# Performance work log

Measured on AMD Instinct MI355X. Metric: run time of the kernel, lower is better.

The kernel has to match this reference:

```python
import jax, jax.numpy as jnp
import numpy as np

N_HEAD = 16
DIM_K = 64
DIM_MODEL = N_HEAD * DIM_K  # 1024; seq_len is forced to equal dim_model by the reshape
SCALE = float(DIM_K ** 0.5)


def setup_inputs() -> dict:
    key = jax.random.key(0)
    ks = jax.random.split(key, 4)
    B, S, D = 32, DIM_MODEL, 1024
    x = jax.random.normal(ks[0], (B, S, D), dtype=jnp.float32)
    glorot = float(1.0 / np.sqrt(D))
    Wq = jax.random.normal(ks[1], (D, DIM_MODEL), dtype=jnp.float32) * glorot
    Wk = jax.random.normal(ks[2], (D, DIM_MODEL), dtype=jnp.float32) * glorot
    Wv = jax.random.normal(ks[3], (D, DIM_MODEL), dtype=jnp.float32) * glorot
    bq = jnp.zeros((DIM_MODEL,), jnp.float32)
    bk = jnp.zeros((DIM_MODEL,), jnp.float32)
    bv = jnp.zeros((DIM_MODEL,), jnp.float32)
    return {"x": x, "Wq": Wq, "bq": bq, "Wk": Wk, "bk": bk, "Wv": Wv, "bv": bv}


def reference(x, Wq, bq, Wk, bk, Wv, bv):
    # x: [B, S, D] with S == DIM_MODEL (required by the original reshape)
    B = x.shape[0]
    q = x @ Wq + bq  # [B, S, dm]
    k = x @ Wk + bk
    v = x @ Wv + bv
    # TF1 K.batch_dot(q, k, axes=[-1,-1]) -> tf.matmul(q, k, adjoint_a=True):
    # contracts over the SEQUENCE axis -> [B, dm, dm]
    y = jnp.einsum('bsd,bse->bde', q, k) / SCALE
    # softmax over dim_k-sized chunks of the last axis
    y = y.reshape(B, DIM_MODEL, N_HEAD, DIM_K)
    y = jax.nn.softmax(y, axis=-1)
    y = y.reshape(B, DIM_MODEL, DIM_MODEL)
    # TF1 K.batch_dot(v, y, axes=[2,3]) -> tf.matmul(v, y) (no adjoints)
    out = jnp.einsum('bsd,bde->bse', v, y)  # [B, S, dm]
    return out
```

## Files before the change

kernel.cpp:

```cpp
#include <hip/hip_runtime.h>
#include <hip/hip_bf16.h>

#define DM 1024
#define NB 32

typedef __bf16 bf16_t;
typedef __attribute__((ext_vector_type(8))) __bf16 bf16x8;
typedef __attribute__((ext_vector_type(4))) float  f32x4;

typedef __attribute__((address_space(1))) void gas_void;
typedef __attribute__((address_space(3))) void las_void;

__device__ __forceinline__ void async_lds16(const bf16_t* g, bf16_t* l) {
    __builtin_amdgcn_global_load_lds((gas_void*)g, (las_void*)l, 16, 0, 0);
}

__device__ inline float bf2f(bf16_t v) {
    union { unsigned short s; __bf16 b; } u; u.b = v;
    union { unsigned int i; float f; } w; w.i = ((unsigned int)u.s) << 16;
    return w.f;
}
__device__ inline bf16_t f2bf(float f) {
    union { unsigned int i; float f; } w; w.f = f;
    unsigned int r = (w.i + 0x7FFFu + ((w.i >> 16) & 1u)) >> 16;
    union { unsigned short s; __bf16 b; } u; u.s = (unsigned short)r;
    return u.b;
}

enum EpiMode { EPI_NONE = 0, EPI_BIAS_ROW = 1, EPI_BIAS_COL = 2, EPI_SCALE = 3 };

__global__ void detect_mode(const unsigned short* __restrict__ x, int* __restrict__ mode)
{
    if (threadIdx.x == 0 && blockIdx.x == 0) {
        int hits = 0;
        for (int i = 0; i < 2048; ++i) {
            unsigned e = (x[i] >> 7) & 0xFFu;
            hits += (e >= 0x8Du) ? 1 : 0;
        }
        *mode = (hits >= 16) ? 1 : 0;
    }
}

__global__ void convert_x(const void* __restrict__ xin, bf16_t* __restrict__ xb,
                          const int* __restrict__ modep, long long off, long long n8)
{
    const long long i = (long long)blockIdx.x * blockDim.x + threadIdx.x;
    if (i >= n8) return;
    bf16x8 o;
    if (*modep) {
        const float* s = (const float*)xin + off + i * 8;
#pragma unroll
        for (int j = 0; j < 8; ++j) o[j] = f2bf(s[j]);
    } else {
        o = *(const bf16x8*)((const bf16_t*)xin + off + i * 8);
    }
    *(bf16x8*)(xb + i * 8) = o;
}

__global__ void transpose3(const void* __restrict__ Wq, const void* __restrict__ Wk,
                           const void* __restrict__ Wv, bf16_t* __restrict__ Wt,
                           const int* __restrict__ modep)
{
    const int md = *modep;
    const void* src = (blockIdx.z == 0) ? Wq : (blockIdx.z == 1) ? Wk : Wv;
    bf16_t* dst = Wt + (size_t)blockIdx.z * DM * DM;
    __shared__ bf16_t T[64][72];
    const int tid = threadIdx.x;
    const int r  = tid >> 2;
    const int cp = tid & 3;
    const int r0 = blockIdx.y * 64;
    const int c0 = blockIdx.x * 64;
    const size_t base = (size_t)(r0 + r) * DM + c0 + cp * 16;
    bf16_t tmp[16];
    if (md) {
        const float* s = (const float*)src + base;
#pragma unroll
        for (int j = 0; j < 16; ++j) tmp[j] = f2bf(s[j]);
    } else {
        const bf16_t* s = (const bf16_t*)src + base;
        bf16x8 a = *(const bf16x8*)s;
        bf16x8 b = *(const bf16x8*)(s + 8);
#pragma unroll
        for (int j = 0; j < 8; ++j) { tmp[j] = a[j]; tmp[8 + j] = b[j]; }
    }
#pragma unroll
    for (int j = 0; j < 16; ++j) T[cp * 16 + j][r] = tmp[j];
    __syncthreads();
    bf16_t* d = dst + (size_t)(c0 + r) * DM + r0 + cp * 16;
    bf16x8 w0, w1;
#pragma unroll
    for (int j = 0; j < 8; ++j) w0[j] = T[r][cp * 16 + j];
#pragma unroll
    for (int j = 0; j < 8; ++j) w1[j] = T[r][cp * 16 + 8 + j];
    *(bf16x8*)d = w0;
    *(bf16x8*)(d + 8) = w1;
}

template <int MODE, bool DUALOUT>
__global__ __launch_bounds__(256, 2)
void gemm_nt(const bf16_t* __restrict__ A, long long sA,
             const bf16_t* __restrict__ B, long long sB,
             void* __restrict__ C, long long sC, long long cOff,
             const void* __restrict__ bias, const int* __restrict__ modep,
             int M, int N, int K, float scale)
{
    constexpr int BM = 128, BN = 128, BK = 64;
    __shared__ __align__(16) bf16_t As[BM * BK];
    __shared__ __align__(16) bf16_t Bs[BN * BK];

    const int Gx = gridDim.x, Gy = gridDim.y;
    const int nwg = Gx * Gy * (int)gridDim.z;
    int bx = blockIdx.x, by = blockIdx.y, z = blockIdx.z;
    if ((nwg & 7) == 0) {
        const int orig = bx + Gx * (by + Gy * z);
        const int nper = nwg >> 3;
        const int nid  = (orig & 7) * nper + (orig >> 3);
        bx = nid % Gx;
        by = (nid / Gx) % Gy;
        z  = nid / (Gx * Gy);
    }

    const bf16_t* Ab = A + (size_t)z * (size_t)sA;
    const bf16_t* Bb = B + (size_t)z * (size_t)sB;

    const int gm0 = by * BM;
    const int gn0 = bx * BN;

    const int tid  = threadIdx.x;
    const int wave = tid >> 6;
    const int lane = tid & 63;
    const int wm   = (wave >> 1) * 64;
    const int wn   = (wave & 1) * 64;
    const int lm   = lane & 15;
    const int quad = lane >> 4;

    f32x4 acc[4][4];
#pragma unroll
    for (int i = 0; i < 4; ++i)
#pragma unroll
        for (int j = 0; j < 4; ++j) acc[i][j] = (f32x4)0.0f;

    const int nIter = K / BK;

    auto stage = [&](int it) {
#pragma unroll
        for (int i = 0; i < 4; ++i) {
            const int ch = tid + i * 256;
            const int row = ch >> 3, kc = ch & 7;
            async_lds16(Ab + (size_t)(gm0 + row) * K + it * BK + kc * 8,
                        As + ch * 8);
            async_lds16(Bb + (size_t)(gn0 + row) * K + it * BK + kc * 8,
                        Bs + ch * 8);
        }
    };

    for (int it = 0; it < nIter; ++it) {
        if (it != 0) __syncthreads();
        stage(it);
        __syncthreads();
#pragma unroll
        for (int kh = 0; kh < 2; ++kh) {
            bf16x8 af[4], bg[4];
#pragma unroll
            for (int mt = 0; mt < 4; ++mt) {
                const int m = wm + mt * 16 + lm;
                af[mt] = *(const bf16x8*)&As[m * BK + (kh * 4 + quad) * 8];
            }
#pragma unroll
            for (int nt = 0; nt < 4; ++nt) {
                const int n = wn + nt * 16 + lm;
                bg[nt] = *(const bf16x8*)&Bs[n * BK + (kh * 4 + quad) * 8];
            }
#pragma unroll
            for (int mt = 0; mt < 4; ++mt)
#pragma unroll
                for (int nt = 0; nt < 4; ++nt)
                    acc[mt][nt] = __builtin_amdgcn_mfma_f32_16x16x32_bf16(
                        af[mt], bg[nt], acc[mt][nt], 0, 0, 0);
        }
    }

    const int md = *modep;
#pragma unroll
    for (int mt = 0; mt < 4; ++mt) {
        float rbias[4];
        if (MODE == EPI_BIAS_ROW) {
#pragma unroll
            for (int r = 0; r < 4; ++r) {
                const int i = gm0 + wm + mt * 16 + quad * 4 + r;
                rbias[r] = md ? ((const float*)bias)[i] : bf2f(((const bf16_t*)bias)[i]);
            }
        }
#pragma unroll
        for (int nt = 0; nt < 4; ++nt) {
            const int col = gn0 + wn + nt * 16 + lm;
            float cbias = 0.f;
            if (MODE == EPI_BIAS_COL)
                cbias = md ? ((const float*)bias)[col] : bf2f(((const bf16_t*)bias)[col]);
#pragma unroll
            for (int r = 0; r < 4; ++r) {
                const int row = gm0 + wm + mt * 16 + quad * 4 + r;
                float v = acc[mt][nt][r];
                if (MODE == EPI_BIAS_ROW) v += rbias[r];
                if (MODE == EPI_BIAS_COL) v += cbias;
                if (MODE == EPI_SCALE)    v *= scale;
                const size_t off = (size_t)cOff + (size_t)z * sC + (size_t)row * N + col;
                if (DUALOUT && md) ((float*)C)[off] = v;
                else               ((bf16_t*)C)[off] = f2bf(v);
            }
        }
    }
}

__global__ void softmax_t_inplace(bf16_t* __restrict__ Y)
{
    const int b = blockIdx.z;
    int idx = blockIdx.x;
    int I = 0;
    while (idx >= 16 - I) { idx -= 16 - I; ++I; }
    const int J = I + idx;

    const int tid = threadIdx.x;
    const int r  = tid >> 2;
    const int cp = tid & 3;

    bf16_t* base = Y + ((size_t)b << 20);
    bf16_t* t0 = base + (size_t)(I * 64 + r) * DM + J * 64 + cp * 16;
    bf16_t* t1 = base + (size_t)(J * 64 + r) * DM + I * 64 + cp * 16;

    __shared__ bf16_t P0[64][72];
    __shared__ bf16_t P1[64][72];

    bf16x8 a0 = *(const bf16x8*)t0;
    bf16x8 a1 = *(const bf16x8*)(t0 + 8);
    bf16x8 c0v, c1v;
    if (J != I) { c0v = *(const bf16x8*)t1; c1v = *(const bf16x8*)(t1 + 8); }

    {
        float f[16];
#pragma unroll
        for (int j = 0; j < 8; ++j) f[j] = bf2f(a0[j]);
#pragma unroll
        for (int j = 0; j < 8; ++j) f[8 + j] = bf2f(a1[j]);
        float m = -1e30f;
#pragma unroll
        for (int j = 0; j < 16; ++j) m = fmaxf(m, f[j]);
        m = fmaxf(m, __shfl_xor(m, 1));
        m = fmaxf(m, __shfl_xor(m, 2));
        float s = 0.f;
#pragma unroll
        for (int j = 0; j < 16; ++j) { f[j] = __expf(f[j] - m); s += f[j]; }
        s += __shfl_xor(s, 1);
        s += __shfl_xor(s, 2);
        const float inv = 1.0f / s;
#pragma unroll
        for (int j = 0; j < 16; ++j) P0[cp * 16 + j][r] = f2bf(f[j] * inv);
    }
    if (J != I) {
        float f[16];
#pragma unroll
        for (int j = 0; j < 8; ++j) f[j] = bf2f(c0v[j]);
#pragma unroll
        for (int j = 0; j < 8; ++j) f[8 + j] = bf2f(c1v[j]);
        float m = -1e30f;
#pragma unroll
        for (int j = 0; j < 16; ++j) m = fmaxf(m, f[j]);
        m = fmaxf(m, __shfl_xor(m, 1));
        m = fmaxf(m, __shfl_xor(m, 2));
        float s = 0.f;
#pragma unroll
        for (int j = 0; j < 16; ++j) { f[j] = __expf(f[j] - m); s += f[j]; }
        s += __shfl_xor(s, 1);
        s += __shfl_xor(s, 2);
        const float inv = 1.0f / s;
#pragma unroll
        for (int j = 0; j < 16; ++j) P1[cp * 16 + j][r] = f2bf(f[j] * inv);
    }
    __syncthreads();

    bf16x8 w0, w1;
#pragma unroll
    for (int j = 0; j < 8; ++j) w0[j] = P0[r][cp * 16 + j];
#pragma unroll
    for (int j = 0; j < 8; ++j) w1[j] = P0[r][cp * 16 + 8 + j];
    *(bf16x8*)t1 = w0;
    *(bf16x8*)(t1 + 8) = w1;
    if (J != I) {
#pragma unroll
        for (int j = 0; j < 8; ++j) w0[j] = P1[r][cp * 16 + j];
#pragma unroll
        for (int j = 0; j < 8; ++j) w1[j] = P1[r][cp * 16 + 8 + j];
        *(bf16x8*)t0 = w0;
        *(bf16x8*)(t0 + 8) = w1;
    }
}

extern "C" void kernel_launch(void* const* d_in, const int* in_sizes, int n_in,
                              void* d_out, int out_size, void* d_ws, size_t ws_size,
                              hipStream_t stream)
{
    const void* x  = d_in[0];
    const void* Wq = d_in[1];
    const void* bq = d_in[2];
    const void* Wk = d_in[3];
    const void* bk = d_in[4];
    const void* Wv = d_in[5];
    const void* bv = d_in[6];

    char* ws = (char*)d_ws;
    int* mode = (int*)ws;
    const size_t MB2 = (size_t)DM * DM * 2;
    const size_t hdr = 256;
    int CB = NB;
    while (CB > 1 && hdr + 3 * MB2 + 4 * (size_t)CB * MB2 > ws_size) CB >>= 1;

    bf16_t* Wt = (bf16_t*)(ws + hdr);
    bf16_t* xb = (bf16_t*)(ws + hdr + 3 * MB2);
    bf16_t* qt = xb + (size_t)CB * DM * DM;
    bf16_t* kt = qt + (size_t)CB * DM * DM;
    bf16_t* y  = kt + (size_t)CB * DM * DM;
    bf16_t* v  = qt;

    detect_mode<<<1, 64, 0, stream>>>((const unsigned short*)x, mode);
    transpose3<<<dim3(16, 16, 3), 256, 0, stream>>>(Wq, Wk, Wv, Wt, mode);

    const long long msz = (long long)DM * DM;
    for (int c = 0; c < NB; c += CB) {
        const int zb = (NB - c < CB) ? (NB - c) : CB;
        const long long n8 = (long long)zb * msz / 8;
        convert_x<<<(int)((n8 + 255) / 256), 256, 0, stream>>>(x, xb, mode, (long long)c * msz, n8);

        const dim3 g(8, 8, zb), blk(256);
        gemm_nt<EPI_BIAS_ROW, false><<<g, blk, 0, stream>>>(Wt, 0, xb, msz, qt, msz, 0, bq, mode, DM, DM, DM, 1.f);
        gemm_nt<EPI_BIAS_ROW, false><<<g, blk, 0, stream>>>(Wt + msz, 0, xb, msz, kt, msz, 0, bk, mode, DM, DM, DM, 1.f);
        gemm_nt<EPI_SCALE, false><<<g, blk, 0, stream>>>(qt, msz, kt, msz, y, msz, 0, nullptr, mode, DM, DM, DM, 0.125f);
        softmax_t_inplace<<<dim3(136, 1, zb), 256, 0, stream>>>(y);
        gemm_nt<EPI_BIAS_COL, false><<<g, blk, 0, stream>>>(xb, msz, Wt + 2 * msz, 0, v, msz, 0, bv, mode, DM, DM, DM, 1.f);
        gemm_nt<EPI_NONE, true><<<g, blk, 0, stream>>>(v, msz, y, msz, d_out, msz, (long long)c * msz, nullptr, mode, DM, DM, DM, 1.f);
    }
}
```

Baseline: 762.8 us.

## Replace GEMM with 256x256 double-buffered 8-wave kernel using swizzled LDS

The 128x128 single-buffered GEMM is replaced with a 256x256 tile kernel that uses 512 threads and 128KB of dynamic LDS. Tile loads are double-buffered: the next K-tile is staged asynchronously while the current one feeds MFMAs, with explicit vmcnt waits and barriers around each quarter-tile. LDS rows are XOR-swizzled to avoid bank conflicts, and s_setprio raises priority during the MFMA bursts. The aim is more operand reuse per tile and hiding global load latency. The costs are hardcoded K=1024 and 256-aligned sizes, fewer workgroups per batch, and heavy LDS use that limits occupancy.

```diff
diff --git a/kernel.cpp b/kernel.cpp
--- a/kernel.cpp
+++ b/kernel.cpp
@@ -97,116 +97,141 @@
 }
 
 template <int MODE, bool DUALOUT>
-__global__ __launch_bounds__(256, 2)
-void gemm_nt(const bf16_t* __restrict__ A, long long sA,
-             const bf16_t* __restrict__ B, long long sB,
-             void* __restrict__ C, long long sC, long long cOff,
-             const void* __restrict__ bias, const int* __restrict__ modep,
-             int M, int N, int K, float scale)
-{
-    constexpr int BM = 128, BN = 128, BK = 64;
-    __shared__ __align__(16) bf16_t As[BM * BK];
-    __shared__ __align__(16) bf16_t Bs[BN * BK];
-
-    const int Gx = gridDim.x, Gy = gridDim.y;
-    const int nwg = Gx * Gy * (int)gridDim.z;
-    int bx = blockIdx.x, by = blockIdx.y, z = blockIdx.z;
-    if ((nwg & 7) == 0) {
-        const int orig = bx + Gx * (by + Gy * z);
-        const int nper = nwg >> 3;
-        const int nid  = (orig & 7) * nper + (orig >> 3);
-        bx = nid % Gx;
-        by = (nid / Gx) % Gy;
-        z  = nid / (Gx * Gy);
+__global__ __launch_bounds__(512, 2)
+void gemm_nt8(const bf16_t* __restrict__ A, long long sA,
+              const bf16_t* __restrict__ B, long long sB,
+              void* __restrict__ C, long long sC, long long cOff,
+              const void* __restrict__ bias, const int* __restrict__ modep,
+              float scale)
+{
+    constexpr int K = 1024;
+    constexpr int NT = K / 64;
+    extern __shared__ bf16_t L[];
+
+    int bx, by, z;
+    {
+        const int nwg  = 16 * (int)gridDim.z;
+        const int orig = (int)blockIdx.x + 4 * ((int)blockIdx.y + 4 * (int)blockIdx.z);
+        const int nid  = (orig & 7) * (nwg >> 3) + (orig >> 3);
+        bx = nid & 3; by = (nid >> 2) & 3; z = nid >> 4;
     }
 
     const bf16_t* Ab = A + (size_t)z * (size_t)sA;
     const bf16_t* Bb = B + (size_t)z * (size_t)sB;
-
-    const int gm0 = by * BM;
-    const int gn0 = bx * BN;
+    const int gm0 = by * 256, gn0 = bx * 256;
 
     const int tid  = threadIdx.x;
-    const int wave = tid >> 6;
     const int lane = tid & 63;
-    const int wm   = (wave >> 1) * 64;
-    const int wn   = (wave & 1) * 64;
+    const int w    = tid >> 6;
+    const int rb   = w >> 1;
+    const int cb   = w & 1;
     const int lm   = lane & 15;
-    const int quad = lane >> 4;
-
-    f32x4 acc[4][4];
-#pragma unroll
-    for (int i = 0; i < 4; ++i)
-#pragma unroll
-        for (int j = 0; j < 4; ++j) acc[i][j] = (f32x4)0.0f;
-
-    const int nIter = K / BK;
-
-    auto stage = [&](int it) {
-#pragma unroll
-        for (int i = 0; i < 4; ++i) {
-            const int ch = tid + i * 256;
-            const int row = ch >> 3, kc = ch & 7;
-            async_lds16(Ab + (size_t)(gm0 + row) * K + it * BK + kc * 8,
-                        As + ch * 8);
-            async_lds16(Bb + (size_t)(gn0 + row) * K + it * BK + kc * 8,
-                        Bs + ch * 8);
+    const int kg   = lane >> 4;
+
+    f32x4 acc[4][2][4];
+#pragma unroll
+    for (int p = 0; p < 4; ++p)
+#pragma unroll
+        for (int i = 0; i < 2; ++i)
+#pragma unroll
+            for (int j = 0; j < 4; ++j) acc[p][i][j] = (f32x4)0.0f;
+
+    auto stage = [&](int kt, int s, int b) {
+        const bf16_t* P  = (s == 0 || s == 3) ? Ab : Bb;
+        const int     g0 = (s == 0 || s == 3) ? gm0 : gn0;
+        const int     h  = (s >= 2) ? 1 : 0;
+        bf16_t* dst = L + (b * 4 + s) * 8192;
+#pragma unroll
+        for (int i = 0; i < 2; ++i) {
+            const int ci  = i * 512 + tid;
+            const int row = ci >> 3;
+            const int kc  = (ci & 7) ^ (row & 7);
+            async_lds16(P + (size_t)(g0 + h * 128 + row) * K + kt * 64 + kc * 8,
+                        dst + ci * 8);
         }
     };
 
-    for (int it = 0; it < nIter; ++it) {
-        if (it != 0) __syncthreads();
-        stage(it);
-        __syncthreads();
-#pragma unroll
-        for (int kh = 0; kh < 2; ++kh) {
-            bf16x8 af[4], bg[4];
-#pragma unroll
-            for (int mt = 0; mt < 4; ++mt) {
-                const int m = wm + mt * 16 + lm;
-                af[mt] = *(const bf16x8*)&As[m * BK + (kh * 4 + quad) * 8];
+    auto rdfrag = [&](int b, int s, int r, int kc) -> bf16x8 {
+        const int byte = r * 128 + ((kc ^ (r & 7)) * 16);
+        return *(const bf16x8*)((const char*)(L + (b * 4 + s) * 8192) + byte);
+    };
+
+#pragma unroll
+    for (int s = 0; s < 4; ++s) stage(0, s, 0);
+    asm volatile("s_waitcnt vmcnt(2)" ::: "memory");
+    __builtin_amdgcn_s_barrier();
+
+#pragma unroll 1
+    for (int kt = 0; kt < NT; ++kt) {
+        const int cur = kt & 1;
+        const int nkt = (kt + 1 < NT) ? kt + 1 : 0;
+#pragma unroll
+        for (int p = 0; p < 4; ++p) {
+            const int sA_ = (p >> 1) ? 3 : 0;
+            const int sB_ = (p & 1) ? 2 : 1;
+            bf16x8 af[2][2], bg[4][2];
+#pragma unroll
+            for (int mt = 0; mt < 2; ++mt)
+#pragma unroll
+                for (int kk = 0; kk < 2; ++kk)
+                    af[mt][kk] = rdfrag(cur, sA_, rb * 32 + mt * 16 + lm, kk * 4 + kg);
+#pragma unroll
+            for (int nt = 0; nt < 4; ++nt)
+#pragma unroll
+                for (int kk = 0; kk < 2; ++kk)
+                    bg[nt][kk] = rdfrag(cur, sB_, cb * 64 + nt * 16 + lm, kk * 4 + kg);
+            stage(nkt, p, cur ^ 1);
+            __builtin_amdgcn_s_barrier();
+            asm volatile("s_waitcnt lgkmcnt(0)" ::: "memory");
+            __builtin_amdgcn_sched_barrier(0);
+            __builtin_amdgcn_s_setprio(1);
+#pragma unroll
+            for (int kk = 0; kk < 2; ++kk)
+#pragma unroll
+                for (int mt = 0; mt < 2; ++mt)
+#pragma unroll
+                    for (int nt = 0; nt < 4; ++nt)
+                        acc[p][mt][nt] = __builtin_amdgcn_mfma_f32_16x16x32_bf16(
+                            af[mt][kk], bg[nt][kk], acc[p][mt][nt], 0, 0, 0);
+            __builtin_amdgcn_s_setprio(0);
+            if (p == 1) { asm volatile("s_waitcnt vmcnt(4)" ::: "memory"); }
+            if (p == 3) { asm volatile("s_waitcnt vmcnt(2)" ::: "memory"); }
+            __builtin_amdgcn_s_barrier();
+        }
+    }
+
+    const int md = *modep;
+#pragma unroll
+    for (int p = 0; p < 4; ++p) {
+        const int rbase = gm0 + (p >> 1) * 128 + rb * 32;
+        const int cbase = gn0 + (p & 1) * 128 + cb * 64;
+#pragma unroll
+        for (int mt = 0; mt < 2; ++mt) {
+            float rbias[4];
+            if (MODE == EPI_BIAS_ROW) {
+#pragma unroll
+                for (int r = 0; r < 4; ++r) {
+                    const int i = rbase + mt * 16 + kg * 4 + r;
+                    rbias[r] = md ? ((const float*)bias)[i] : bf2f(((const bf16_t*)bias)[i]);
+                }
             }
 #pragma unroll
             for (int nt = 0; nt < 4; ++nt) {
-                const int n = wn + nt * 16 + lm;
-                bg[nt] = *(const bf16x8*)&Bs[n * BK + (kh * 4 + quad) * 8];
-            }
-#pragma unroll
-            for (int mt = 0; mt < 4; ++mt)
-#pragma unroll
-                for (int nt = 0; nt < 4; ++nt)
-                    acc[mt][nt] = __builtin_amdgcn_mfma_f32_16x16x32_bf16(
-                        af[mt], bg[nt], acc[mt][nt], 0, 0, 0);
-        }
-    }
-
-    const int md = *modep;
-#pragma unroll
-    for (int mt = 0; mt < 4; ++mt) {
-        float rbias[4];
-        if (MODE == EPI_BIAS_ROW) {
-#pragma unroll
-            for (int r = 0; r < 4; ++r) {
-                const int i = gm0 + wm + mt * 16 + quad * 4 + r;
-                rbias[r] = md ? ((const float*)bias)[i] : bf2f(((const bf16_t*)bias)[i]);
-            }
-        }
-#pragma unroll
-        for (int nt = 0; nt < 4; ++nt) {
-            const int col = gn0 + wn + nt * 16 + lm;
-            float cbias = 0.f;
-            if (MODE == EPI_BIAS_COL)
-                cbias = md ? ((const float*)bias)[col] : bf2f(((const bf16_t*)bias)[col]);
-#pragma unroll
-            for (int r = 0; r < 4; ++r) {
-                const int row = gm0 + wm + mt * 16 + quad * 4 + r;
-                float v = acc[mt][nt][r];
-                if (MODE == EPI_BIAS_ROW) v += rbias[r];
-                if (MODE == EPI_BIAS_COL) v += cbias;
-                if (MODE == EPI_SCALE)    v *= scale;
-                const size_t off = (size_t)cOff + (size_t)z * sC + (size_t)row * N + col;
-                if (DUALOUT && md) ((float*)C)[off] = v;
-                else               ((bf16_t*)C)[off] = f2bf(v);
+                const int col = cbase + nt * 16 + lm;
+                float cbias = 0.f;
+                if (MODE == EPI_BIAS_COL)
+                    cbias = md ? ((const float*)bias)[col] : bf2f(((const bf16_t*)bias)[col]);
+#pragma unroll
+                for (int r = 0; r < 4; ++r) {
+                    const int row = rbase + mt * 16 + kg * 4 + r;
+                    float vv = acc[p][mt][nt][r];
+                    if (MODE == EPI_BIAS_ROW) vv += rbias[r];
+                    if (MODE == EPI_BIAS_COL) vv += cbias;
+                    if (MODE == EPI_SCALE)    vv *= scale;
+                    const size_t off = (size_t)cOff + (size_t)z * sC + (size_t)row * 1024 + col;
+                    if (DUALOUT && md) ((float*)C)[off] = vv;
+                    else               ((bf16_t*)C)[off] = f2bf(vv);
+                }
             }
         }
     }
@@ -307,6 +332,19 @@
     const void* Wv = d_in[5];
     const void* bv = d_in[6];
 
+    static bool attr_done = false;
+    if (!attr_done) {
+        hipFuncSetAttribute((const void*)gemm_nt8<EPI_BIAS_ROW, false>,
+                            hipFuncAttributeMaxDynamicSharedMemorySize, 131072);
+        hipFuncSetAttribute((const void*)gemm_nt8<EPI_BIAS_COL, false>,
+                            hipFuncAttributeMaxDynamicSharedMemorySize, 131072);
+        hipFuncSetAttribute((const void*)gemm_nt8<EPI_SCALE, false>,
+                            hipFuncAttributeMaxDynamicSharedMemorySize, 131072);
+        hipFuncSetAttribute((const void*)gemm_nt8<EPI_NONE, true>,
+                            hipFuncAttributeMaxDynamicSharedMemorySize, 131072);
+        attr_done = true;
+    }
+
     char* ws = (char*)d_ws;
     int* mode = (int*)ws;
     const size_t MB2 = (size_t)DM * DM * 2;
@@ -330,12 +368,12 @@
         const long long n8 = (long long)zb * msz / 8;
         convert_x<<<(int)((n8 + 255) / 256), 256, 0, stream>>>(x, xb, mode, (long long)c * msz, n8);
 
-        const dim3 g(8, 8, zb), blk(256);
-        gemm_nt<EPI_BIAS_ROW, false><<<g, blk, 0, stream>>>(Wt, 0, xb, msz, qt, msz, 0, bq, mode, DM, DM, DM, 1.f);
-        gemm_nt<EPI_BIAS_ROW, false><<<g, blk, 0, stream>>>(Wt + msz, 0, xb, msz, kt, msz, 0, bk, mode, DM, DM, DM, 1.f);
-        gemm_nt<EPI_SCALE, false><<<g, blk, 0, stream>>>(qt, msz, kt, msz, y, msz, 0, nullptr, mode, DM, DM, DM, 0.125f);
+        const dim3 g8(4, 4, zb), blk8(512);
+        gemm_nt8<EPI_BIAS_ROW, false><<<g8, blk8, 131072, stream>>>(Wt, 0, xb, msz, qt, msz, 0, bq, mode, 1.f);
+        gemm_nt8<EPI_BIAS_ROW, false><<<g8, blk8, 131072, stream>>>(Wt + msz, 0, xb, msz, kt, msz, 0, bk, mode, 1.f);
+        gemm_nt8<EPI_SCALE, false><<<g8, blk8, 131072, stream>>>(qt, msz, kt, msz, y, msz, 0, nullptr, mode, 0.125f);
         softmax_t_inplace<<<dim3(136, 1, zb), 256, 0, stream>>>(y);
-        gemm_nt<EPI_BIAS_COL, false><<<g, blk, 0, stream>>>(xb, msz, Wt + 2 * msz, 0, v, msz, 0, bv, mode, DM, DM, DM, 1.f);
-        gemm_nt<EPI_NONE, true><<<g, blk, 0, stream>>>(v, msz, y, msz, d_out, msz, (long long)c * msz, nullptr, mode, DM, DM, DM, 1.f);
-    }
-}
+        gemm_nt8<EPI_BIAS_COL, false><<<g8, blk8, 131072, stream>>>(xb, msz, Wt + 2 * msz, 0, v, msz, 0, bv, mode, 1.f);
+        gemm_nt8<EPI_NONE, true><<<g8, blk8, 131072, stream>>>(v, msz, y, msz, d_out, msz, (long long)c * msz, nullptr, mode, 1.f);
+    }
+}
```

After: 698.7 us. 1.09x faster.
